# Performance work log

Hardware: AMD Instinct MI355X
Metric: run time of the kernel (lower is better)

The kernel has to match this reference:

```python
import jax, jax.numpy as jnp
import numpy as np

# Fixed 6-node graph from the module (source -> target, PyG convention)
SRC = jnp.array([1, 2, 0, 2, 1, 3, 2, 4, 3, 5, 3, 4], dtype=jnp.int32)
DST = jnp.array([0, 0, 1, 1, 2, 2, 3, 3, 4, 4, 5, 5], dtype=jnp.int32)
N_NODES = 6
FEAT = 64
BATCH = 131072


def _gcn_norm(fill_value):
    # add self loops with weight fill_value (improved=True -> 2.0)
    src = jnp.concatenate([SRC, jnp.arange(N_NODES, dtype=jnp.int32)])
    dst = jnp.concatenate([DST, jnp.arange(N_NODES, dtype=jnp.int32)])
    w = jnp.concatenate([jnp.ones(12, jnp.float32), jnp.full((N_NODES,), fill_value, jnp.float32)])
    deg = jnp.zeros((N_NODES,), jnp.float32).at[dst].add(w)
    dinv = jnp.where(deg > 0, jax.lax.rsqrt(deg), 0.0)
    norm = dinv[src] * w * dinv[dst]  # [18]
    return src, dst, norm


def _gcn_conv(x, W, b, fill_value):
    # x: [B, N, F]; PyG GCNConv: h = x @ W^T, aggregate norm * h[src] at dst, add bias
    h = jnp.einsum('bnf,gf->bng', x, W)
    src, dst, norm = _gcn_norm(fill_value)
    msg = h[:, src, :] * norm[None, :, None]          # [B, 18, F]
    out = jnp.zeros_like(h).at[:, dst, :].add(msg)     # scatter-add over targets
    return out + b


def setup_inputs() -> dict:
    key = jax.random.key(0)
    ks = jax.random.split(key, 12)
    s = 1.0 / np.sqrt(FEAT)
    inp = {'x': jax.random.normal(ks[0], (BATCH, N_NODES, FEAT), jnp.float32)}
    for i in range(4):
        inp[f'W{i+1}'] = jax.random.uniform(ks[1 + 2 * i], (FEAT, FEAT), jnp.float32, -s, s)
        inp[f'b{i+1}'] = jax.random.uniform(ks[2 + 2 * i], (FEAT,), jnp.float32, -s, s)
    inp['fc_w'] = jax.random.uniform(ks[9], (N_NODES, FEAT), jnp.float32, -s, s)  # 6 stacked Linear(64,1) weights
    inp['fc_b'] = jax.random.uniform(ks[10], (N_NODES,), jnp.float32, -s, s)
    return inp


def reference(x, W1, b1, W2, b2, W3, b3, W4, b4, fc_w, fc_b):
    h = jax.nn.relu(_gcn_conv(x, W1, b1, 1.0))
    h = jax.nn.relu(_gcn_conv(h, W2, b2, 1.0))
    h = jax.nn.relu(_gcn_conv(h, W3, b3, 2.0))  # improved=True
    h = jax.nn.relu(_gcn_conv(h, W4, b4, 2.0))  # improved=True
    r = h + x  # residual
    # per-node Linear(64,1) heads, concatenated -> [B, 6]
    logits = jnp.einsum('bnf,nf->bn', r, fc_w) + fc_b
    return jax.nn.sigmoid(logits)
```

## Files before the change

### kernel.cpp

```cpp
#include <hip/hip_runtime.h>

typedef __attribute__((ext_vector_type(8))) _Float16 f16x8;
typedef __attribute__((ext_vector_type(4))) _Float16 f16x4;
typedef __attribute__((ext_vector_type(2))) __fp16 fp16x2;
typedef __attribute__((ext_vector_type(4))) float f32x4;

union U8 { f16x8 v; fp16x2 p[4]; };
union U4 { f16x4 v; fp16x2 p[2]; };

__device__ __forceinline__ f16x8 cvt8(f32x4 a, f32x4 b) {
  U8 u;
  u.p[0] = __builtin_amdgcn_cvt_pkrtz(a.x, a.y);
  u.p[1] = __builtin_amdgcn_cvt_pkrtz(a.z, a.w);
  u.p[2] = __builtin_amdgcn_cvt_pkrtz(b.x, b.y);
  u.p[3] = __builtin_amdgcn_cvt_pkrtz(b.z, b.w);
  return u.v;
}
__device__ __forceinline__ f16x4 cvt4(f32x4 a) {
  U4 u;
  u.p[0] = __builtin_amdgcn_cvt_pkrtz(a.x, a.y);
  u.p[1] = __builtin_amdgcn_cvt_pkrtz(a.z, a.w);
  return u.v;
}
__device__ __forceinline__ float dot4(f32x4 a, f32x4 b) {
  return a.x * b.x + a.y * b.y + a.z * b.z + a.w * b.w;
}

#define BT 32

__global__ __launch_bounds__(256, 4) void gcn_fused(
    const float* __restrict__ x,
    const float* __restrict__ W1, const float* __restrict__ B1,
    const float* __restrict__ W2, const float* __restrict__ B2,
    const float* __restrict__ W3, const float* __restrict__ B3,
    const float* __restrict__ W4, const float* __restrict__ B4,
    const float* __restrict__ fcw, const float* __restrict__ fcb,
    float* __restrict__ out)
{
  __shared__ __align__(16) _Float16 xs[6 * BT * 64];
  __shared__ float pacc_s[6][BT];
  __shared__ float ls[BT][6];

  const int tid  = threadIdx.x;
  const int lane = tid & 63;
  const int w    = tid >> 6;
  const int c    = lane & 15;
  const int q    = lane >> 4;
  const int b0   = blockIdx.x * BT;

  const int CONS[6][4] = {{0,1,-1,-1},{0,1,2,-1},{0,1,2,3},{2,3,4,5},{3,4,5,-1},{4,5,-1,-1}};
  const float* Ws[4] = {W1, W2, W3, W4};
  const float* Bs[4] = {B1, B2, B3, B4};

  {
    const float* xb = x + (size_t)b0 * 384;
#pragma unroll
    for (int r = 0; r < 6; ++r) {
      const int i = tid * 8 + r * 2048;
      const int b = i / 384;
      const int rem = i - b * 384;
      const int n = rem >> 6;
      const int f = rem & 63;
      f32x4 v0 = *(const f32x4*)(xb + i);
      f32x4 v1 = *(const f32x4*)(xb + i + 4);
      const float* fw = fcw + n * 64 + f;
      float p = dot4(v0, *(const f32x4*)fw) + dot4(v1, *(const f32x4*)(fw + 4));
      p += __shfl_xor(p, 1, 64);
      p += __shfl_xor(p, 2, 64);
      p += __shfl_xor(p, 4, 64);
      if ((tid & 7) == 0) pacc_s[n][b] = p;
      const int slot = (f >> 3) ^ (b & 7);
      *(f16x8*)&xs[(n * BT + b) * 64 + slot * 8] = cvt8(v0, v1);
    }
  }
  __syncthreads();

  f32x4 acc[2][6];
  const int s1 = (q ^ (c & 7)) * 8;
  const int s2 = ((q + 4) ^ (c & 7)) * 8;
  const int wsl = ((w * 2 + (q >> 1)) ^ (c & 7)) * 8 + (q & 1) * 4;

#pragma unroll
  for (int l = 0; l < 4; ++l) {
    const float cbv = (l < 2) ? (1.f / 3.f) : 0.25f;
    const float* wp = Ws[l] + (w * 16 + c) * 64 + q * 8;
    f32x4 u0 = *(const f32x4*)wp        * cbv;
    f32x4 u1 = *(const f32x4*)(wp + 4)  * cbv;
    f32x4 u2 = *(const f32x4*)(wp + 32) * cbv;
    f32x4 u3 = *(const f32x4*)(wp + 36) * cbv;
    f16x8 wb0 = cvt8(u0, u1), wb1 = cvt8(u2, u3);
    f16x8 wa0, wa1;
    if (l < 2) { wa0 = wb0; wa1 = wb1; }
    else       { wa0 = wb0 + wb0; wa1 = wb1 + wb1; }
    const f32x4 bval = *(const f32x4*)(Bs[l] + w * 16 + q * 4);
#pragma unroll
    for (int hh = 0; hh < 2; ++hh)
#pragma unroll
      for (int n = 0; n < 6; ++n) acc[hh][n] = bval;

#pragma unroll
    for (int m = 0; m < 6; ++m) {
#pragma unroll
      for (int hh = 0; hh < 2; ++hh) {
        const int row = (m * BT + hh * 16 + c) * 64;
        f16x8 a0 = *(const f16x8*)&xs[row + s1];
        f16x8 a1 = *(const f16x8*)&xs[row + s2];
#pragma unroll
        for (int j = 0; j < 4; ++j) {
          const int n = CONS[m][j];
          if (n >= 0) {
            acc[hh][n] = __builtin_amdgcn_mfma_f32_16x16x32_f16((n == m) ? wa0 : wb0, a0, acc[hh][n], 0, 0, 0);
            acc[hh][n] = __builtin_amdgcn_mfma_f32_16x16x32_f16((n == m) ? wa1 : wb1, a1, acc[hh][n], 0, 0, 0);
          }
        }
      }
    }
    __syncthreads();
#pragma unroll
    for (int hh = 0; hh < 2; ++hh) {
      const int brow = hh * 16 + c;
#pragma unroll
      for (int n = 0; n < 6; ++n) {
        f32x4 r;
#pragma unroll
        for (int e = 0; e < 4; ++e) r[e] = fmaxf(acc[hh][n][e], 0.f);
        *(f16x4*)&xs[(n * BT + brow) * 64 + wsl] = cvt4(r);
      }
    }
    __syncthreads();
  }

  const f32x4 z4 = {0.f, 0.f, 0.f, 0.f};
#pragma unroll
  for (int u = w; u < 12; u += 4) {
    const int n = u % 6;
    const int hh = u / 6;
    const int row = (n * BT + hh * 16 + c) * 64;
    f16x8 hb0 = *(const f16x8*)&xs[row + s1];
    f16x8 hb1 = *(const f16x8*)&xs[row + s2];
    const float* fw = fcw + n * 64 + q * 8;
    f16x8 fa0 = cvt8(*(const f32x4*)fw,        *(const f32x4*)(fw + 4));
    f16x8 fa1 = cvt8(*(const f32x4*)(fw + 32), *(const f32x4*)(fw + 36));
    f32x4 sv = __builtin_amdgcn_mfma_f32_16x16x32_f16(fa0, hb0, z4, 0, 0, 0);
    sv = __builtin_amdgcn_mfma_f32_16x16x32_f16(fa1, hb1, sv, 0, 0, 0);
    if (q == 0) {
      const float v = sv[0] + pacc_s[n][hh * 16 + c] + fcb[n];
      ls[hh * 16 + c][n] = 1.f / (1.f + __expf(-v));
    }
  }
  __syncthreads();
  if (tid < 192) out[(size_t)b0 * 6 + tid] = ((const float*)ls)[tid];
}

extern "C" void kernel_launch(void* const* d_in, const int* in_sizes, int n_in,
                              void* d_out, int out_size, void* d_ws, size_t ws_size,
                              hipStream_t stream) {
  const float* x   = (const float*)d_in[0];
  const float* W1  = (const float*)d_in[1];
  const float* B1  = (const float*)d_in[2];
  const float* W2  = (const float*)d_in[3];
  const float* B2  = (const float*)d_in[4];
  const float* W3  = (const float*)d_in[5];
  const float* B3  = (const float*)d_in[6];
  const float* W4  = (const float*)d_in[7];
  const float* B4  = (const float*)d_in[8];
  const float* fcw = (const float*)d_in[9];
  const float* fcb = (const float*)d_in[10];
  float* out = (float*)d_out;

  const int batch  = in_sizes[0] / (6 * 64);
  const int blocks = batch / BT;
  hipLaunchKernelGGL(gcn_fused, dim3(blocks), dim3(256), 0, stream,
                     x, W1, B1, W2, B2, W3, B3, W4, B4, fcw, fcb, out);
}
```

Baseline: 77.59 us.

## Compute H=XW once per node, aggregate neighbors in registers, double-buffer LDS

Each layer now runs one 64x64 MFMA product per node and forms the normalized neighbor sum from the per-node results in registers. Before, the kernel ran a separate MFMA for each incoming edge with the weights pre-scaled. Block size drops to 16 batch rows, weight fragments for all layers are hoisted into registers up front, and the activations use a ping-pong LDS buffer so only one barrier per layer is needed. This cuts MFMA work by roughly 3x, at the cost of more register pressure from the hoisted weights and twice as many smaller blocks.

Result: slower. 101.9 us (+31.4%).

```diff
diff --git a/kernel.cpp b/kernel.cpp
--- a/kernel.cpp
+++ b/kernel.cpp
@@ -26,7 +26,7 @@
   return a.x * b.x + a.y * b.y + a.z * b.z + a.w * b.w;
 }
 
-#define BT 32
+#define BT 16
 
 __global__ __launch_bounds__(256, 4) void gcn_fused(
     const float* __restrict__ x,
@@ -37,7 +37,7 @@
     const float* __restrict__ fcw, const float* __restrict__ fcb,
     float* __restrict__ out)
 {
-  __shared__ __align__(16) _Float16 xs[6 * BT * 64];
+  __shared__ __align__(16) _Float16 xs[2][6 * BT * 64];
   __shared__ float pacc_s[6][BT];
   __shared__ float ls[BT][6];
 
@@ -48,14 +48,25 @@
   const int q    = lane >> 4;
   const int b0   = blockIdx.x * BT;
 
-  const int CONS[6][4] = {{0,1,-1,-1},{0,1,2,-1},{0,1,2,3},{2,3,4,5},{3,4,5,-1},{4,5,-1,-1}};
-  const float* Ws[4] = {W1, W2, W3, W4};
-  const float* Bs[4] = {B1, B2, B3, B4};
+  const float* Wg[4] = {W1, W2, W3, W4};
+  const float* Bg[4] = {B1, B2, B3, B4};
+  const int NB0[6] = {1, 0, 1, 2, 3, 3};
+  const int NB1[6] = {2, 2, 3, 4, 5, 4};
+  const f32x4 z4 = {0.f, 0.f, 0.f, 0.f};
+
+  f16x8 wfr[4][2];
+#pragma unroll
+  for (int l = 0; l < 4; ++l)
+#pragma unroll
+    for (int kf = 0; kf < 2; ++kf) {
+      const float* wp = Wg[l] + (w * 16 + c) * 64 + kf * 32 + q * 8;
+      wfr[l][kf] = cvt8(*(const f32x4*)wp, *(const f32x4*)(wp + 4));
+    }
 
   {
     const float* xb = x + (size_t)b0 * 384;
 #pragma unroll
-    for (int r = 0; r < 6; ++r) {
+    for (int r = 0; r < 3; ++r) {
       const int i = tid * 8 + r * 2048;
       const int b = i / 384;
       const int rem = i - b * 384;
@@ -70,86 +81,64 @@
       p += __shfl_xor(p, 4, 64);
       if ((tid & 7) == 0) pacc_s[n][b] = p;
       const int slot = (f >> 3) ^ (b & 7);
-      *(f16x8*)&xs[(n * BT + b) * 64 + slot * 8] = cvt8(v0, v1);
+      *(f16x8*)&xs[0][(n * BT + b) * 64 + slot * 8] = cvt8(v0, v1);
     }
   }
   __syncthreads();
 
-  f32x4 acc[2][6];
-  const int s1 = (q ^ (c & 7)) * 8;
-  const int s2 = ((q + 4) ^ (c & 7)) * 8;
+  const int s1  = (q ^ (c & 7)) * 8;
+  const int s2  = ((q + 4) ^ (c & 7)) * 8;
   const int wsl = ((w * 2 + (q >> 1)) ^ (c & 7)) * 8 + (q & 1) * 4;
 
+  int cur = 0;
 #pragma unroll
   for (int l = 0; l < 4; ++l) {
-    const float cbv = (l < 2) ? (1.f / 3.f) : 0.25f;
-    const float* wp = Ws[l] + (w * 16 + c) * 64 + q * 8;
-    f32x4 u0 = *(const f32x4*)wp        * cbv;
-    f32x4 u1 = *(const f32x4*)(wp + 4)  * cbv;
-    f32x4 u2 = *(const f32x4*)(wp + 32) * cbv;
-    f32x4 u3 = *(const f32x4*)(wp + 36) * cbv;
-    f16x8 wb0 = cvt8(u0, u1), wb1 = cvt8(u2, u3);
-    f16x8 wa0, wa1;
-    if (l < 2) { wa0 = wb0; wa1 = wb1; }
-    else       { wa0 = wb0 + wb0; wa1 = wb1 + wb1; }
-    const f32x4 bval = *(const f32x4*)(Bs[l] + w * 16 + q * 4);
-#pragma unroll
-    for (int hh = 0; hh < 2; ++hh)
-#pragma unroll
-      for (int n = 0; n < 6; ++n) acc[hh][n] = bval;
-
+    const f32x4 bval = *(const f32x4*)(Bg[l] + w * 16 + q * 4);
+    f32x4 acc[6];
 #pragma unroll
     for (int m = 0; m < 6; ++m) {
+      const _Float16* rp = &xs[cur][(m * BT + c) * 64];
+      f16x8 a0 = *(const f16x8*)&rp[s1];
+      f16x8 a1 = *(const f16x8*)&rp[s2];
+      f32x4 d = __builtin_amdgcn_mfma_f32_16x16x32_f16(wfr[l][0], a0, z4, 0, 0, 0);
+      acc[m]  = __builtin_amdgcn_mfma_f32_16x16x32_f16(wfr[l][1], a1, d, 0, 0, 0);
+    }
+    cur ^= 1;
 #pragma unroll
-      for (int hh = 0; hh < 2; ++hh) {
-        const int row = (m * BT + hh * 16 + c) * 64;
-        f16x8 a0 = *(const f16x8*)&xs[row + s1];
-        f16x8 a1 = *(const f16x8*)&xs[row + s2];
+    for (int n = 0; n < 6; ++n) {
+      f32x4 t;
+      if (l < 2) {
 #pragma unroll
-        for (int j = 0; j < 4; ++j) {
-          const int n = CONS[m][j];
-          if (n >= 0) {
-            acc[hh][n] = __builtin_amdgcn_mfma_f32_16x16x32_f16((n == m) ? wa0 : wb0, a0, acc[hh][n], 0, 0, 0);
-            acc[hh][n] = __builtin_amdgcn_mfma_f32_16x16x32_f16((n == m) ? wa1 : wb1, a1, acc[hh][n], 0, 0, 0);
-          }
-        }
+        for (int e = 0; e < 4; ++e)
+          t[e] = (acc[n][e] + acc[NB0[n]][e] + acc[NB1[n]][e]) * (1.f / 3.f) + bval[e];
+      } else {
+#pragma unroll
+        for (int e = 0; e < 4; ++e)
+          t[e] = 0.5f * acc[n][e] + 0.25f * (acc[NB0[n]][e] + acc[NB1[n]][e]) + bval[e];
       }
-    }
-    __syncthreads();
 #pragma unroll
-    for (int hh = 0; hh < 2; ++hh) {
-      const int brow = hh * 16 + c;
-#pragma unroll
-      for (int n = 0; n < 6; ++n) {
-        f32x4 r;
-#pragma unroll
-        for (int e = 0; e < 4; ++e) r[e] = fmaxf(acc[hh][n][e], 0.f);
-        *(f16x4*)&xs[(n * BT + brow) * 64 + wsl] = cvt4(r);
-      }
+      for (int e = 0; e < 4; ++e) t[e] = fmaxf(t[e], 0.f);
+      *(f16x4*)&xs[cur][(n * BT + c) * 64 + wsl] = cvt4(t);
     }
     __syncthreads();
   }
 
-  const f32x4 z4 = {0.f, 0.f, 0.f, 0.f};
-#pragma unroll
-  for (int u = w; u < 12; u += 4) {
-    const int n = u % 6;
-    const int hh = u / 6;
-    const int row = (n * BT + hh * 16 + c) * 64;
-    f16x8 hb0 = *(const f16x8*)&xs[row + s1];
-    f16x8 hb1 = *(const f16x8*)&xs[row + s2];
+  for (int n = w; n < 6; n += 4) {
+    const _Float16* rp = &xs[0][(n * BT + c) * 64];
+    f16x8 hb0 = *(const f16x8*)&rp[s1];
+    f16x8 hb1 = *(const f16x8*)&rp[s2];
     const float* fw = fcw + n * 64 + q * 8;
     f16x8 fa0 = cvt8(*(const f32x4*)fw,        *(const f32x4*)(fw + 4));
     f16x8 fa1 = cvt8(*(const f32x4*)(fw + 32), *(const f32x4*)(fw + 36));
     f32x4 sv = __builtin_amdgcn_mfma_f32_16x16x32_f16(fa0, hb0, z4, 0, 0, 0);
     sv = __builtin_amdgcn_mfma_f32_16x16x32_f16(fa1, hb1, sv, 0, 0, 0);
     if (q == 0) {
-      const float v = sv[0] + pacc_s[n][hh * 16 + c] + fcb[n];
-      ls[hh * 16 + c][n] = 1.f / (1.f + __expf(-v));
+      const float v = sv[0] + pacc_s[n][c] + fcb[n];
+      ls[c][n] = 1.f / (1.f + __expf(-v));
     }
   }
   __syncthreads();
-  if (tid < 192) out[(size_t)b0 * 6 + tid] = ((const float*)ls)[tid];
+  if (tid < 96) out[(size_t)b0 * 6 + tid] = ((const float*)ls)[tid];
 }
 
 extern "C" void kernel_launch(void* const* d_in, const int* in_sizes, int n_in,
@@ -168,7 +157,7 @@
   const float* fcb = (const float*)d_in[10];
   float* out = (float*)d_out;
 
-  const int batch  = in_sizes[0] / (6 * 64);
+  const int batch  = in_sizes[0] / 384;
   const int blocks = batch / BT;
   hipLaunchKernelGGL(gcn_fused, dim3(blocks), dim3(256), 0, stream,
                      x, W1, B1, W2, B2, W3, B3, W4, B4, fcw, fcb, out);
```
